# Kernel optimization log

Measured on AMD Instinct MI355X. Metric: run time of the kernel, lower is better.

## Reference

```python
import jax, jax.numpy as jnp
import numpy as np
from jax import lax

T, B, D_IN, D_DAY, H, D_OUT = 64, 32, 4096, 256, 256, 942


def setup_inputs() -> dict:
    key = jax.random.key(0)
    ks = jax.random.split(key, 18)
    s = 0.05
    def rn(k, shape):
        return jax.random.normal(k, shape, jnp.float32) * s
    return {
        "x": jax.random.uniform(ks[0], (T, B, D_IN), jnp.float32),
        "W_emb": rn(ks[1], (D_DAY, D_IN)), "b_emb": rn(ks[2], (D_DAY,)),
        "Wih_f": rn(ks[3], (3 * H, D_DAY)), "Whh_f": rn(ks[4], (3 * H, H)),
        "bih_f": rn(ks[5], (3 * H,)), "bhh_f": rn(ks[6], (3 * H,)),
        "Wih_r": rn(ks[7], (3 * H, D_DAY)), "Whh_r": rn(ks[8], (3 * H, H)),
        "bih_r": rn(ks[9], (3 * H,)), "bhh_r": rn(ks[10], (3 * H,)),
        "attn_w": rn(ks[11], (2 * H,)), "attn_b": rn(ks[12], ()),
        "W_ao": rn(ks[13], (D_DAY, 4 * H)), "b_ao": rn(ks[14], (D_DAY,)),
        "W_o": rn(ks[15], (D_OUT, D_DAY)), "b_o": rn(ks[16], (D_OUT,)),
    }


def _gru_cell(xt, h, Wih, Whh, bih, bhh):
    # PyTorch nn.GRU cell math
    gi = xt @ Wih.T + bih          # [B, 3H]
    gh = h @ Whh.T + bhh           # [B, 3H]
    ir, iz, inn = jnp.split(gi, 3, axis=-1)
    hr, hz, hn = jnp.split(gh, 3, axis=-1)
    r = jax.nn.sigmoid(ir + hr)
    z = jax.nn.sigmoid(iz + hz)
    n = jnp.tanh(inn + r * hn)
    return (1.0 - z) * n + z * h


def _run_gru(seq, Wih, Whh, bih, bhh):
    # seq: [L, B, D] -> all hidden states [L, B, H], h0 = zeros
    h0 = jnp.zeros((seq.shape[1], H), seq.dtype)
    def step(h, xt):
        h2 = _gru_cell(xt, h, Wih, Whh, bih, bhh)
        return h2, h2
    return lax.scan(step, h0, seq)[1]


def reference(x, W_emb, b_emb, Wih_f, Whh_f, bih_f, bhh_f,
              Wih_r, Whh_r, bih_r, bhh_r, attn_w, attn_b,
              W_ao, b_ao, W_o, b_o):
    day_emb = jnp.einsum('tbi,di->tbd', x, W_emb) + b_emb       # [T,B,Dday]

    # Forward GRU over the prefix [:i+1] equals the first i+1 states of one full run.
    fwd = _run_gru(day_emb, Wih_f, Whh_f, bih_f, bhh_f)          # [T,B,H]

    # Reverse GRU is recomputed per timestep on the flipped prefix (O(T^2)).
    i_idx = jnp.arange(T)
    j_idx = jnp.arange(T)
    gather = jnp.clip(i_idx[:, None] - j_idx[None, :], 0)        # [T,T]
    rev_in = day_emb[gather]                                     # [T,T,B,Dday]; row i, step j = day_emb[i-j]
    rev = jax.vmap(lambda s: _run_gru(s, Wih_r, Whh_r, bih_r, bhh_r))(rev_in)  # [T,T,B,H]

    # Attention scores on concat(fwd, rev) without materializing the 2H concat:
    w_f, w_r = attn_w[:H], attn_w[H:]
    scores = (jnp.einsum('tbh,h->tb', fwd, w_f)[None, :, :]
              + jnp.einsum('itbh,h->itb', rev, w_r) + attn_b)    # [T(i),T(t),B]
    valid = j_idx[None, :] <= i_idx[:, None]                     # t <= i
    scores = jnp.where(valid[:, :, None], scores, -jnp.inf)
    alpha = jax.nn.softmax(scores, axis=1)                       # softmax over prefix time

    counts = (i_idx + 1).astype(day_emb.dtype)[:, None, None]    # mean over i+1 steps
    c_fwd = jnp.einsum('itb,tbh->ibh', alpha, fwd) / counts      # [T,B,H]
    c_rev = jnp.einsum('itb,itbh->ibh', alpha, rev) / counts     # [T,B,H]
    rev_last = rev[i_idx, i_idx]                                 # rnn_h[-1] reverse half, [T,B,H]

    h_t = jnp.concatenate([c_fwd, c_rev, fwd, rev_last], axis=-1)  # [T,B,4H]
    h_t_out = h_t @ W_ao.T + b_ao                                # [T,B,Dday]
    return jax.nn.sigmoid(h_t_out @ W_o.T + b_o)                 # [T,B,D_OUT]
```

## Files before the change

kernel.cpp:

```cpp
#include <hip/hip_runtime.h>
#include <hip/hip_bf16.h>


typedef __bf16 bf16x8 __attribute__((ext_vector_type(8)));
typedef __bf16 bf16x4 __attribute__((ext_vector_type(4)));
typedef float  f32x4  __attribute__((ext_vector_type(4)));
typedef int    int4v  __attribute__((ext_vector_type(4)));

static constexpr float NEG_L2E = -1.442695041f;
static constexpr float TWO_L2E =  2.885390082f;

static constexpr size_t OFF_PK_EMB = 0;
static constexpr size_t OFF_PK_IH  = 2097152;
static constexpr size_t OFF_WQ     = 2883584;
static constexpr size_t OFF_WSC    = 3276800;
static constexpr size_t OFF_PK_AO  = 3670016;
static constexpr size_t OFF_PK_O   = 4194304;
static constexpr size_t OFF_DAY    = 4685824;
static constexpr size_t OFF_GIT    = 5734400;
static constexpr size_t OFF_BC     = 12025856;
static constexpr size_t OFF_REV    = 18317312;
static constexpr size_t OFF_FWD    = 52396032;
static constexpr size_t OFF_HT     = 53444608;
static constexpr size_t OFF_TMP1   = 57638912;
static constexpr size_t OFF_XB     = OFF_REV;

__device__ __forceinline__ float sigf(float x) {
    return __builtin_amdgcn_rcpf(1.f + __expf(-x));
}

#define LDS_BARRIER() asm volatile("s_waitcnt lgkmcnt(0)\n\ts_barrier" ::: "memory")

__global__ __launch_bounds__(256) void pack_misc(
    const float* __restrict__ We,  const float* __restrict__ Wir, const float* __restrict__ Wif,
    const float* __restrict__ Wao, const float* __restrict__ Wo,  const float* __restrict__ x,
    const float* __restrict__ Whr, const float* __restrict__ Whf,
    const float* __restrict__ bih_r, const float* __restrict__ bih_f,
    const float* __restrict__ bhh_r, const float* __restrict__ bhh_f,
    __bf16* pe, __bf16* pi, __bf16* pao, __bf16* po, __bf16* xb,
    signed char* __restrict__ wq, float* __restrict__ wscale, float* __restrict__ bc)
{
    int b = blockIdx.x;
    if (b >= 5048) {
        int rowb = (b - 5048) * 4 + (threadIdx.x >> 6);
        int t = threadIdx.x & 63;
        int dir = (rowb >= 768) ? 1 : 0;
        int n = rowb - dir * 768;
        const float* src = (dir ? Whf : Whr) + (size_t)n * 256;
        float4 wv = ((const float4*)src)[t];
        float m = fmaxf(fmaxf(fabsf(wv.x), fabsf(wv.y)), fmaxf(fabsf(wv.z), fabsf(wv.w)));
#pragma unroll
        for (int off = 32; off > 0; off >>= 1) m = fmaxf(m, __shfl_xor(m, off));
        m = fmaxf(m, 1e-20f);
        float inv = 127.f / m;
        int q0 = (int)__builtin_rintf(wv.x * inv);
        int q1 = (int)__builtin_rintf(wv.y * inv);
        int q2 = (int)__builtin_rintf(wv.z * inv);
        int q3 = (int)__builtin_rintf(wv.w * inv);
        int pk = (q0 & 0xff) | ((q1 & 0xff) << 8) | ((q2 & 0xff) << 16) | ((q3 & 0xff) << 24);
        int dlane = (n & 15) | (((t >> 2) & 3) << 4);
        size_t byte = (size_t)dir * 196608 + ((size_t)(n >> 4) * 4 + (t >> 4)) * 1024
                    + (size_t)dlane * 16 + (t & 3) * 4;
        *(int*)(wq + byte) = pk;
        if (t == 0) {
            float gc = (n < 512) ? NEG_L2E : TWO_L2E;
            wscale[rowb] = m * (1.f / 16129.f) * gc;
            const float* bi = dir ? bih_f : bih_r;
            const float* bh = dir ? bhh_f : bhh_r;
            bc[rowb] = (n < 512) ? (bi[n] + bh[n]) * NEG_L2E : bi[n] * TWO_L2E;
        }
        return;
    }
    if (b >= 952) {
        size_t base = ((size_t)(b - 952) * 256 + threadIdx.x) * 8;
        float4 v0 = *(const float4*)(x + base);
        float4 v1 = *(const float4*)(x + base + 4);
        bf16x8 o;
        o[0]=(__bf16)v0.x; o[1]=(__bf16)v0.y; o[2]=(__bf16)v0.z; o[3]=(__bf16)v0.w;
        o[4]=(__bf16)v1.x; o[5]=(__bf16)v1.y; o[6]=(__bf16)v1.z; o[7]=(__bf16)v1.w;
        *(bf16x8*)(xb + base) = o;
        return;
    }
    const float* src; __bf16* dst; int Nsrc, k32l, b0; bool ih = false;
    if (b < 512)      { src = We;  dst = pe;          Nsrc = 256; k32l = 7; b0 = 0;   }
    else if (b < 608) { src = Wir; dst = pi;          Nsrc = 768; k32l = 3; b0 = 512; ih = true; }
    else if (b < 704) { src = Wif; dst = pi + 196608; Nsrc = 768; k32l = 3; b0 = 608; ih = true; }
    else if (b < 832) { src = Wao; dst = pao;         Nsrc = 256; k32l = 5; b0 = 704; }
    else              { src = Wo;  dst = po;          Nsrc = 942; k32l = 3; b0 = 832; }
    int t8   = (b - b0) * 256 + threadIdx.x;
    int lane = t8 & 63;
    int K32  = 1 << k32l;
    int K    = K32 << 5;
    int ks   = (t8 >> 6) & (K32 - 1);
    int nt   = t8 >> (6 + k32l);
    int n    = nt * 16 + (lane & 15);
    int k0   = ks * 32 + ((lane >> 4) << 3);
    bf16x8 o;
    if (n < Nsrc) {
        const float* sp = src + (size_t)n * K + k0;
        float4 v0 = *(const float4*)sp;
        float4 v1 = *(const float4*)(sp + 4);
        float s = ih ? ((n < 512) ? NEG_L2E : TWO_L2E) : 1.f;
        o[0]=(__bf16)(v0.x*s); o[1]=(__bf16)(v0.y*s); o[2]=(__bf16)(v0.z*s); o[3]=(__bf16)(v0.w*s);
        o[4]=(__bf16)(v1.x*s); o[5]=(__bf16)(v1.y*s); o[6]=(__bf16)(v1.z*s); o[7]=(__bf16)(v1.w*s);
    } else {
#pragma unroll
        for (int q = 0; q < 8; q++) o[q] = (__bf16)0.f;
    }
    *(bf16x8*)(dst + (size_t)t8 * 8) = o;
}

template<int MODE, int KDIM, int NTILES, int CSTRIDE, int NREAL>
__global__ __launch_bounds__(256) void gemm_k(
    const __bf16* __restrict__ Ap, const __bf16* __restrict__ Bp, void* __restrict__ Cp,
    const float* __restrict__ bias)
{
    __shared__ __align__(16) __bf16 As[32][88];
    const int tid = threadIdx.x;
    const int w = tid >> 6, lane = tid & 63, c = lane & 15, quad = lane >> 4;
    const int mb = blockIdx.x, nb = blockIdx.y;
    constexpr int K32 = KDIM / 32;
    constexpr int NK  = KDIM / 64;
    constexpr int NT_W = NTILES / 2;
    const int wrow = w & 1, ncol0 = (w >> 1) * NT_W;

    f32x4 acc[NT_W];
#pragma unroll
    for (int nt = 0; nt < NT_W; nt++) acc[nt] = (f32x4){0.f, 0.f, 0.f, 0.f};

    const int row = tid >> 3, kp = (tid & 7) * 8;
    uint4 pb;
    auto issue  = [&](int kb) { pb = *(const uint4*)(Ap + (size_t)(mb * 32 + row) * KDIM + kb * 64 + kp); };
    auto commit = [&]() { *(uint4*)&As[row][kp] = pb; };

    bf16x8 bcur[2][NT_W], bnxt[2][NT_W];
    auto loadB = [&](int kb, bf16x8 (&dst)[2][NT_W]) {
#pragma unroll
        for (int kk = 0; kk < 2; kk++)
#pragma unroll
            for (int nt = 0; nt < NT_W; nt++)
                dst[kk][nt] = *(const bf16x8*)(Bp +
                    ((size_t)((nb * NTILES + ncol0 + nt) * K32 + kb * 2 + kk) * 64 + lane) * 8);
    };

    issue(0);
    loadB(0, bcur);
    for (int kb = 0; kb < NK; kb++) {
        commit();
        __syncthreads();
        if (kb + 1 < NK) { issue(kb + 1); loadB(kb + 1, bnxt); }
#pragma unroll
        for (int kk = 0; kk < 2; kk++) {
            bf16x8 a = *(const bf16x8*)&As[wrow * 16 + c][kk * 32 + quad * 8];
#pragma unroll
            for (int nt = 0; nt < NT_W; nt++)
                acc[nt] = __builtin_amdgcn_mfma_f32_16x16x32_bf16(a, bcur[kk][nt], acc[nt], 0, 0, 0);
        }
        if (kb + 1 < NK) {
#pragma unroll
            for (int kk = 0; kk < 2; kk++)
#pragma unroll
                for (int nt = 0; nt < NT_W; nt++) bcur[kk][nt] = bnxt[kk][nt];
        }
        __syncthreads();
    }

#pragma unroll
    for (int nt = 0; nt < NT_W; nt++) {
        int n = nb * (NTILES * 16) + (ncol0 + nt) * 16 + c;
        float bv = (n < NREAL) ? bias[n] : 0.f;
#pragma unroll
        for (int r0 = 0; r0 < 4; r0++) {
            int m = mb * 32 + wrow * 16 + quad * 4 + r0;
            float v = acc[nt][r0] + bv;
            if constexpr (MODE == 0) ((__bf16*)Cp)[(size_t)m * CSTRIDE + n] = (__bf16)v;
            else { if (n < NREAL) ((float*)Cp)[(size_t)m * CSTRIDE + n] = sigf(v); }
        }
    }
}

__device__ __forceinline__ void gru_cell4(
    const int4v a0, const int4v a1, const int4v a2,
    const f32x4 sc0, const f32x4 sc1, const f32x4 sc2, const f32x4 bnv,
    const bf16x4 g0, const bf16x4 g1, const bf16x4 g2,
    float* hreg, int* pk, bf16x4* hb)
{
    float f[4];
#pragma unroll
    for (int r = 0; r < 4; r++) {
        float er = __builtin_amdgcn_exp2f(fmaf((float)a0[r], sc0[r], (float)g0[r]));
        float rg = __builtin_amdgcn_rcpf(1.f + er);
        float ez = __builtin_amdgcn_exp2f(fmaf((float)a1[r], sc1[r], (float)g1[r]));
        float zg = __builtin_amdgcn_rcpf(1.f + ez);
        float narg = fmaf(rg, fmaf((float)a2[r], sc2[r], bnv[r]), (float)g2[r]);
        float en = __builtin_amdgcn_exp2f(narg);
        float ng = fmaf(-2.f, __builtin_amdgcn_rcpf(1.f + en), 1.f);
        float h  = fmaf(zg, hreg[r] - ng, ng);
        hreg[r] = h;
        (*hb)[r] = (__bf16)h;
        f[r] = fmaf(h, 127.f, 12582912.f);
    }
    unsigned lo = __builtin_amdgcn_perm(__float_as_uint(f[1]), __float_as_uint(f[0]), 0x00000400u);
    unsigned hi = __builtin_amdgcn_perm(__float_as_uint(f[3]), __float_as_uint(f[2]), 0x04000000u);
    *pk = (int)__builtin_amdgcn_perm(hi, lo, 0x07060100u);
}

__global__ __launch_bounds__(512, 2) void gru_recurrent(
    const signed char* __restrict__ wq, const float* __restrict__ wscale,
    const float* __restrict__ bhh_r, const float* __restrict__ bhh_f,
    const __bf16* __restrict__ Gi,
    __bf16* __restrict__ revb, __bf16* __restrict__ fwdb)
{
    __shared__ __align__(16) signed char hbuf[2][4096];
    const int tid = threadIdx.x;
    const int w = tid >> 6, lane = tid & 63, c = lane & 15, quad = lane >> 4;
    const int bid = blockIdx.x;
    const bool isF = (bid < 2);
    const int ia = isF ? 63 : (63 - ((bid - 2) >> 1));
    const int b0 = (bid & 1) << 4;
    const int steps = ia + 1;
    const float* bhh = isF ? bhh_f : bhh_r;
    __bf16* outb = isF ? fwdb : (revb + ((size_t)(ia * (ia + 1) / 2)) * 8192);
    const int dirb = isF ? 768 : 0;

    const int4v* pw = (const int4v*)(wq + (isF ? 196608 : 0));
    int4v bw[3][2][4];
#pragma unroll
    for (int g = 0; g < 3; g++)
#pragma unroll
        for (int mt = 0; mt < 2; mt++)
#pragma unroll
            for (int ks = 0; ks < 4; ks++)
                bw[g][mt][ks] = pw[(size_t)((g * 16 + 2 * w + mt) * 4 + ks) * 64 + lane];

    const int d0 = (w << 5) + (quad << 2);
    const int d1 = d0 + 16;
    f32x4 sc[3][2], bnv[2];
#pragma unroll
    for (int g = 0; g < 3; g++)
#pragma unroll
        for (int mt = 0; mt < 2; mt++)
            sc[g][mt] = *(const f32x4*)&wscale[dirb + g * 256 + d0 + 16 * mt];
#pragma unroll
    for (int mt = 0; mt < 2; mt++) {
        bnv[mt] = *(const f32x4*)&bhh[512 + d0 + 16 * mt];
#pragma unroll
        for (int q = 0; q < 4; q++) bnv[mt][q] *= TWO_L2E;
    }

    float hreg[8] = {0.f, 0.f, 0.f, 0.f, 0.f, 0.f, 0.f, 0.f};
    ((int*)hbuf)[tid]        = 0; ((int*)hbuf)[tid + 512]  = 0;
    ((int*)hbuf)[tid + 1024] = 0; ((int*)hbuf)[tid + 1536] = 0;
    __syncthreads();

    const __bf16* grow = Gi + (size_t)((isF ? 0 : ia) * 32 + b0 + c) * 1536 + dirb;
    const long gstep = isF ? (32 * 1536) : -(32 * 1536);
    __bf16* go = outb + (size_t)(b0 + c) * 256 + d0;

    const int wr0 = ((d0 >> 6) << 10) + ((c | (((d0 >> 4) & 3) << 4)) << 4) + (d0 & 15);
    const int wr1 = ((d1 >> 6) << 10) + ((c | (((d1 >> 4) & 3) << 4)) << 4) + (d1 & 15);
    const int rd_off = lane << 4;

    bf16x4 gc[3][2];
#pragma unroll
    for (int g = 0; g < 3; g++)
#pragma unroll
        for (int mt = 0; mt < 2; mt++)
            gc[g][mt] = *(const bf16x4*)(grow + g * 256 + d0 + 16 * mt);

    for (int j = 0; j < steps; j++) {
        const int rb = j & 1, wbuf = rb ^ 1;
        const bool more = (j + 1 < steps);

        int4v acc[3][2];
#pragma unroll
        for (int g = 0; g < 3; g++)
#pragma unroll
            for (int mt = 0; mt < 2; mt++) acc[g][mt] = (int4v){0, 0, 0, 0};
#pragma unroll
        for (int ks = 0; ks < 4; ks++) {
            int4v av = *(const int4v*)&hbuf[rb][ks * 1024 + rd_off];
#pragma unroll
            for (int g = 0; g < 3; g++) {
                acc[g][0] = __builtin_amdgcn_mfma_i32_16x16x64_i8(bw[g][0][ks], av, acc[g][0], 0, 0, 0);
                acc[g][1] = __builtin_amdgcn_mfma_i32_16x16x64_i8(bw[g][1][ks], av, acc[g][1], 0, 0, 0);
            }
        }

        int pk0, pk1; bf16x4 hb0, hb1;
        gru_cell4(acc[0][0], acc[1][0], acc[2][0], sc[0][0], sc[1][0], sc[2][0], bnv[0],
                  gc[0][0], gc[1][0], gc[2][0], &hreg[0], &pk0, &hb0);
        gru_cell4(acc[0][1], acc[1][1], acc[2][1], sc[0][1], sc[1][1], sc[2][1], bnv[1],
                  gc[0][1], gc[1][1], gc[2][1], &hreg[4], &pk1, &hb1);

        *(int*)&hbuf[wbuf][wr0] = pk0;
        *(int*)&hbuf[wbuf][wr1] = pk1;

        if (more) {
            grow += gstep;
#pragma unroll
            for (int g = 0; g < 3; g++)
#pragma unroll
                for (int mt = 0; mt < 2; mt++)
                    gc[g][mt] = *(const bf16x4*)(grow + g * 256 + d0 + 16 * mt);
        }

        *(bf16x4*)go = hb0;
        *(bf16x4*)(go + 16) = hb1;
        go += 8192;
        LDS_BARRIER();
    }
}

__global__ __launch_bounds__(512) void attn_kernel(
    const __bf16* __restrict__ revb, const __bf16* __restrict__ fwdb,
    const float* __restrict__ attn_w, const float* __restrict__ attn_bp,
    __bf16* __restrict__ ht)
{
    const int tid = threadIdx.x;
    const int w = tid >> 6, lane = tid & 63;
    const int wid = blockIdx.x * 8 + w;
    const int i = wid >> 5, b = wid & 31;
    const int d0 = lane * 4;

    float wf[4], wr[4];
#pragma unroll
    for (int q = 0; q < 4; q++) { wf[q] = attn_w[d0 + q]; wr[q] = attn_w[256 + d0 + q]; }
    const float ab = attn_bp[0];
    const __bf16* rp = revb + ((size_t)(i * (i + 1) / 2)) * 8192 + (size_t)b * 256 + d0;
    const __bf16* fp = fwdb + (size_t)b * 256 + d0;

    float mx = -1e30f, l = 0.f;
    float cf[4] = {0,0,0,0}, cr[4] = {0,0,0,0};
    bf16x4 rn = *(const bf16x4*)rp, fn = *(const bf16x4*)fp;
    for (int t = 0; t <= i; t++) {
        bf16x4 rv4 = rn, fv4 = fn;
        if (t < i) {
            rn = *(const bf16x4*)(rp + (size_t)(t + 1) * 8192);
            fn = *(const bf16x4*)(fp + (size_t)(t + 1) * 8192);
        }
        float rv[4], fv[4], s = 0.f;
#pragma unroll
        for (int q = 0; q < 4; q++) {
            rv[q] = (float)rv4[q]; fv[q] = (float)fv4[q];
            s += rv[q] * wr[q] + fv[q] * wf[q];
        }
#pragma unroll
        for (int off = 32; off > 0; off >>= 1) s += __shfl_xor(s, off);
        s += ab;
        float mn = fmaxf(mx, s);
        float scl = __expf(mx - mn);
        float p  = __expf(s - mn);
        l = l * scl + p;
#pragma unroll
        for (int q = 0; q < 4; q++) { cf[q] = cf[q] * scl + p * fv[q]; cr[q] = cr[q] * scl + p * rv[q]; }
        mx = mn;
    }
    float inv = __builtin_amdgcn_rcpf(l * (float)(i + 1));
    __bf16* hp = ht + (size_t)(i * 32 + b) * 1024 + d0;
    const __bf16* fl = fp + (size_t)i * 8192;
    const __bf16* rl = rp + (size_t)i * 8192;
#pragma unroll
    for (int q = 0; q < 4; q++) {
        hp[q]       = (__bf16)(cf[q] * inv);
        hp[256 + q] = (__bf16)(cr[q] * inv);
        hp[512 + q] = fl[q];
        hp[768 + q] = rl[q];
    }
}

extern "C" void kernel_launch(void* const* d_in, const int* in_sizes, int n_in,
                              void* d_out, int out_size, void* d_ws, size_t ws_size,
                              hipStream_t stream) {
    const float* x      = (const float*)d_in[0];
    const float* W_emb  = (const float*)d_in[1];
    const float* b_emb  = (const float*)d_in[2];
    const float* Wih_f  = (const float*)d_in[3];
    const float* Whh_f  = (const float*)d_in[4];
    const float* bih_f  = (const float*)d_in[5];
    const float* bhh_f  = (const float*)d_in[6];
    const float* Wih_r  = (const float*)d_in[7];
    const float* Whh_r  = (const float*)d_in[8];
    const float* bih_r  = (const float*)d_in[9];
    const float* bhh_r  = (const float*)d_in[10];
    const float* attn_w = (const float*)d_in[11];
    const float* attn_b = (const float*)d_in[12];
    const float* W_ao   = (const float*)d_in[13];
    const float* b_ao   = (const float*)d_in[14];
    const float* W_o    = (const float*)d_in[15];
    const float* b_o    = (const float*)d_in[16];
    float* out = (float*)d_out;

    char* ws = (char*)d_ws;
    __bf16* pk_emb = (__bf16*)(ws + OFF_PK_EMB);
    __bf16* pk_ih  = (__bf16*)(ws + OFF_PK_IH);
    signed char* wq = (signed char*)(ws + OFF_WQ);
    float*  wsc    = (float*)(ws + OFF_WSC);
    __bf16* pk_ao  = (__bf16*)(ws + OFF_PK_AO);
    __bf16* pk_o   = (__bf16*)(ws + OFF_PK_O);
    __bf16* day    = (__bf16*)(ws + OFF_DAY);
    __bf16* Gi     = (__bf16*)(ws + OFF_GIT);
    float*  bc     = (float*)(ws + OFF_BC);
    __bf16* revb   = (__bf16*)(ws + OFF_REV);
    __bf16* fwdb   = (__bf16*)(ws + OFF_FWD);
    __bf16* ht     = (__bf16*)(ws + OFF_HT);
    __bf16* tmp1   = (__bf16*)(ws + OFF_TMP1);
    __bf16* xb     = (__bf16*)(ws + OFF_XB);

    pack_misc<<<5432, 256, 0, stream>>>(W_emb, Wih_r, Wih_f, W_ao, W_o, x,
                                        Whh_r, Whh_f, bih_r, bih_f, bhh_r, bhh_f,
                                        pk_emb, pk_ih, pk_ao, pk_o, xb, wq, wsc, bc);

    gemm_k<0, 4096, 2, 256, 256><<<dim3(64, 8), 256, 0, stream>>>(xb, pk_emb, day, b_emb);
    gemm_k<0, 256, 4, 1536, 1536><<<dim3(64, 24), 256, 0, stream>>>(day, pk_ih, Gi, bc);

    gru_recurrent<<<130, 512, 0, stream>>>(wq, wsc, bhh_r, bhh_f, Gi, revb, fwdb);

    attn_kernel<<<256, 512, 0, stream>>>(revb, fwdb, attn_w, attn_b, ht);

    gemm_k<0, 1024, 2, 256, 256><<<dim3(64, 8), 256, 0, stream>>>(ht, pk_ao, tmp1, b_ao);
    gemm_k<1, 256, 4, 942, 942><<<dim3(64, 15), 256, 0, stream>>>(tmp1, pk_o, out, b_o);
}
```

Baseline: 308.4 us.

## Halve GRU recurrent block to 4 waves, each covering 64 hidden units

The recurrent GRU kernel now runs 256 threads (4 waves) per block instead of 512. Each wave handles four 16-row M-tiles per gate instead of two, so it keeps twice as many int8 weight fragments and accumulators in registers. The aim is to cut the per-step barrier cost and LDS traffic in the latency-bound sequential loop by syncing fewer waves. In exchange, each wave issues twice as many MFMAs in series per step, and register pressure rises (48 weight vectors plus 12 accumulators), which could lead to spills.

```diff
diff --git a/kernel.cpp b/kernel.cpp
--- a/kernel.cpp
+++ b/kernel.cpp
@@ -205,7 +205,7 @@
     *pk = (int)__builtin_amdgcn_perm(hi, lo, 0x07060100u);
 }
 
-__global__ __launch_bounds__(512, 2) void gru_recurrent(
+__global__ __launch_bounds__(256, 1) void gru_recurrent(
     const signed char* __restrict__ wq, const float* __restrict__ wscale,
     const float* __restrict__ bhh_r, const float* __restrict__ bhh_f,
     const __bf16* __restrict__ Gi,
@@ -224,89 +224,92 @@
     const int dirb = isF ? 768 : 0;
 
     const int4v* pw = (const int4v*)(wq + (isF ? 196608 : 0));
-    int4v bw[3][2][4];
+    int4v bw[3][4][4];
 #pragma unroll
     for (int g = 0; g < 3; g++)
 #pragma unroll
-        for (int mt = 0; mt < 2; mt++)
+        for (int mt = 0; mt < 4; mt++)
 #pragma unroll
             for (int ks = 0; ks < 4; ks++)
-                bw[g][mt][ks] = pw[(size_t)((g * 16 + 2 * w + mt) * 4 + ks) * 64 + lane];
-
-    const int d0 = (w << 5) + (quad << 2);
-    const int d1 = d0 + 16;
-    f32x4 sc[3][2], bnv[2];
+                bw[g][mt][ks] = pw[(size_t)((g * 16 + 4 * w + mt) * 4 + ks) * 64 + lane];
+
+    const int db = (w << 6) + (quad << 2);
+    f32x4 sc[3][4], bnv[4];
 #pragma unroll
     for (int g = 0; g < 3; g++)
 #pragma unroll
-        for (int mt = 0; mt < 2; mt++)
-            sc[g][mt] = *(const f32x4*)&wscale[dirb + g * 256 + d0 + 16 * mt];
-#pragma unroll
-    for (int mt = 0; mt < 2; mt++) {
-        bnv[mt] = *(const f32x4*)&bhh[512 + d0 + 16 * mt];
+        for (int mt = 0; mt < 4; mt++)
+            sc[g][mt] = *(const f32x4*)&wscale[dirb + g * 256 + db + 16 * mt];
+#pragma unroll
+    for (int mt = 0; mt < 4; mt++) {
+        bnv[mt] = *(const f32x4*)&bhh[512 + db + 16 * mt];
 #pragma unroll
         for (int q = 0; q < 4; q++) bnv[mt][q] *= TWO_L2E;
     }
 
-    float hreg[8] = {0.f, 0.f, 0.f, 0.f, 0.f, 0.f, 0.f, 0.f};
-    ((int*)hbuf)[tid]        = 0; ((int*)hbuf)[tid + 512]  = 0;
-    ((int*)hbuf)[tid + 1024] = 0; ((int*)hbuf)[tid + 1536] = 0;
+    float hreg[16];
+#pragma unroll
+    for (int q = 0; q < 16; q++) hreg[q] = 0.f;
+#pragma unroll
+    for (int q = 0; q < 8; q++) ((int*)hbuf)[tid + q * 256] = 0;
     __syncthreads();
 
-    const __bf16* grow = Gi + (size_t)((isF ? 0 : ia) * 32 + b0 + c) * 1536 + dirb;
+    const __bf16* grow = Gi + (size_t)((isF ? 0 : ia) * 32 + b0 + c) * 1536 + dirb + db;
     const long gstep = isF ? (32 * 1536) : -(32 * 1536);
-    __bf16* go = outb + (size_t)(b0 + c) * 256 + d0;
-
-    const int wr0 = ((d0 >> 6) << 10) + ((c | (((d0 >> 4) & 3) << 4)) << 4) + (d0 & 15);
-    const int wr1 = ((d1 >> 6) << 10) + ((c | (((d1 >> 4) & 3) << 4)) << 4) + (d1 & 15);
+    __bf16* go = outb + (size_t)(b0 + c) * 256 + db;
+
+    int wr[4];
+#pragma unroll
+    for (int mt = 0; mt < 4; mt++) wr[mt] = (w << 10) + ((c | (mt << 4)) << 4) + (quad << 2);
     const int rd_off = lane << 4;
 
-    bf16x4 gc[3][2];
+    bf16x4 gc[3][4];
 #pragma unroll
     for (int g = 0; g < 3; g++)
 #pragma unroll
-        for (int mt = 0; mt < 2; mt++)
-            gc[g][mt] = *(const bf16x4*)(grow + g * 256 + d0 + 16 * mt);
+        for (int mt = 0; mt < 4; mt++)
+            gc[g][mt] = *(const bf16x4*)(grow + g * 256 + 16 * mt);
 
     for (int j = 0; j < steps; j++) {
         const int rb = j & 1, wbuf = rb ^ 1;
         const bool more = (j + 1 < steps);
 
-        int4v acc[3][2];
+        int4v acc[3][4];
 #pragma unroll
         for (int g = 0; g < 3; g++)
 #pragma unroll
-            for (int mt = 0; mt < 2; mt++) acc[g][mt] = (int4v){0, 0, 0, 0};
+            for (int mt = 0; mt < 4; mt++) acc[g][mt] = (int4v){0, 0, 0, 0};
 #pragma unroll
         for (int ks = 0; ks < 4; ks++) {
             int4v av = *(const int4v*)&hbuf[rb][ks * 1024 + rd_off];
 #pragma unroll
-            for (int g = 0; g < 3; g++) {
-                acc[g][0] = __builtin_amdgcn_mfma_i32_16x16x64_i8(bw[g][0][ks], av, acc[g][0], 0, 0, 0);
-                acc[g][1] = __builtin_amdgcn_mfma_i32_16x16x64_i8(bw[g][1][ks], av, acc[g][1], 0, 0, 0);
-            }
-        }
-
-        int pk0, pk1; bf16x4 hb0, hb1;
-        gru_cell4(acc[0][0], acc[1][0], acc[2][0], sc[0][0], sc[1][0], sc[2][0], bnv[0],
-                  gc[0][0], gc[1][0], gc[2][0], &hreg[0], &pk0, &hb0);
-        gru_cell4(acc[0][1], acc[1][1], acc[2][1], sc[0][1], sc[1][1], sc[2][1], bnv[1],
-                  gc[0][1], gc[1][1], gc[2][1], &hreg[4], &pk1, &hb1);
-
-        *(int*)&hbuf[wbuf][wr0] = pk0;
-        *(int*)&hbuf[wbuf][wr1] = pk1;
+            for (int g = 0; g < 3; g++)
+#pragma unroll
+                for (int mt = 0; mt < 4; mt++)
+                    acc[g][mt] = __builtin_amdgcn_mfma_i32_16x16x64_i8(bw[g][mt][ks], av, acc[g][mt], 0, 0, 0);
+        }
+
+        int pk[4]; bf16x4 hb[4];
+#pragma unroll
+        for (int mt = 0; mt < 4; mt++) {
+            gru_cell4(acc[0][mt], acc[1][mt], acc[2][mt],
+                      sc[0][mt], sc[1][mt], sc[2][mt], bnv[mt],
+                      gc[0][mt], gc[1][mt], gc[2][mt], &hreg[4 * mt], &pk[mt], &hb[mt]);
+            *(int*)&hbuf[wbuf][wr[mt]] = pk[mt];
+        }
 
         if (more) {
             grow += gstep;
 #pragma unroll
             for (int g = 0; g < 3; g++)
 #pragma unroll
-                for (int mt = 0; mt < 2; mt++)
-                    gc[g][mt] = *(const bf16x4*)(grow + g * 256 + d0 + 16 * mt);
-        }
-
-        *(bf16x4*)go = hb0;
-        *(bf16x4*)(go + 16) = hb1;
+                for (int mt = 0; mt < 4; mt++)
+                    gc[g][mt] = *(const bf16x4*)(grow + g * 256 + 16 * mt);
+        }
+
+#pragma unroll
+        for (int mt = 0; mt < 4; mt++)
+            *(bf16x4*)(go + 16 * mt) = hb[mt];
         go += 8192;
         LDS_BARRIER();
     }
@@ -414,7 +417,7 @@
     gemm_k<0, 4096, 2, 256, 256><<<dim3(64, 8), 256, 0, stream>>>(xb, pk_emb, day, b_emb);
     gemm_k<0, 256, 4, 1536, 1536><<<dim3(64, 24), 256, 0, stream>>>(day, pk_ih, Gi, bc);
 
-    gru_recurrent<<<130, 512, 0, stream>>>(wq, wsc, bhh_r, bhh_f, Gi, revb, fwdb);
+    gru_recurrent<<<130, 256, 0, stream>>>(wq, wsc, bhh_r, bhh_f, Gi, revb, fwdb);
 
     attn_kernel<<<256, 512, 0, stream>>>(revb, fwdb, attn_w, attn_b, ht);
 
```

After: 360.9 us. +17.0%, slower.
